# Optimization experiments

Measured on AMD Instinct MI355X. Metric: run time of the kernel, lower is better.

Reference implementation:

```python
import jax, jax.numpy as jnp
import numpy as np
import math

HIDDEN = 1024
HEADS = 16
D_K = HIDDEN // HEADS
D_FF = 4 * HIDDEN
EPS = 1e-5


def gelu_tanh(x):
    # exact match of the module's hand-written GELU
    c = math.sqrt(2.0 / math.pi)
    return 0.5 * x * (1.0 + jnp.tanh(c * (x + 0.044715 * x ** 3)))


def layer_norm(x, gamma, beta):
    mu = jnp.mean(x, axis=-1, keepdims=True)
    var = jnp.mean((x - mu) ** 2, axis=-1, keepdims=True)
    return (x - mu) * jax.lax.rsqrt(var + EPS) * gamma + beta


def setup_inputs() -> dict:
    key = jax.random.key(0)
    ks = jax.random.split(key, 16)
    s = 0.02
    B, S, H = 4, 2048, HIDDEN
    return {
        "x": jax.random.normal(ks[0], (B, S, H), dtype=jnp.float32),
        "Wq": jax.random.normal(ks[1], (H, H), dtype=jnp.float32) * s,
        "bq": jnp.zeros((H,), jnp.float32),
        "Wk": jax.random.normal(ks[2], (H, H), dtype=jnp.float32) * s,
        "bk": jnp.zeros((H,), jnp.float32),
        "Wv": jax.random.normal(ks[3], (H, H), dtype=jnp.float32) * s,
        "bv": jnp.zeros((H,), jnp.float32),
        "Wo": jax.random.normal(ks[4], (H, H), dtype=jnp.float32) * s,
        "bo": jnp.zeros((H,), jnp.float32),
        "W1": jax.random.normal(ks[5], (H, D_FF), dtype=jnp.float32) * s,
        "b1": jnp.zeros((D_FF,), jnp.float32),
        "W2": jax.random.normal(ks[6], (D_FF, H), dtype=jnp.float32) * s,
        "b2": jnp.zeros((H,), jnp.float32),
        "g1": jnp.ones((H,), jnp.float32),
        "be1": jnp.zeros((H,), jnp.float32),
        "g2": jnp.ones((H,), jnp.float32),
        "be2": jnp.zeros((H,), jnp.float32),
    }


def reference(x, Wq, bq, Wk, bk, Wv, bv, Wo, bo, W1, b1, W2, b2, g1, be1, g2, be2):
    B, S, H = x.shape
    # QKV projections -> [B, heads, S, d_k]
    def split_heads(t):
        return t.reshape(B, S, HEADS, D_K).transpose(0, 2, 1, 3)
    q = split_heads(x @ Wq + bq)
    k = split_heads(x @ Wk + bk)
    v = split_heads(x @ Wv + bv)
    scores = jnp.einsum("bhsd,bhtd->bhst", q, k) / math.sqrt(D_K)
    attn = jax.nn.softmax(scores, axis=-1)
    ctx = jnp.einsum("bhst,bhtd->bhsd", attn, v)
    ctx = ctx.transpose(0, 2, 1, 3).reshape(B, S, H)
    attn_out = ctx @ Wo + bo
    x = layer_norm(x + attn_out, g1, be1)
    ff = gelu_tanh(x @ W1 + b1) @ W2 + b2
    x = layer_norm(x + ff, g2, be2)
    return x
```

## Files before the change

kernel.cpp:

```cpp
#include <hip/hip_runtime.h>
#include <hip/hip_bf16.h>
#include <math.h>

#define HIDDEN 1024
#define NHEADS 16
#define DK 64
#define DFF 4096
#define SEQ 2048
#define NBATCH 4
#define NTOK (NBATCH*SEQ)

typedef __attribute__((ext_vector_type(8))) short bf16x8;
typedef __attribute__((ext_vector_type(4))) float f32x4;
typedef __attribute__((ext_vector_type(16))) float f32x16;
typedef __attribute__((ext_vector_type(4))) unsigned short us4;
typedef __attribute__((ext_vector_type(2))) unsigned int u32x2;

typedef __attribute__((address_space(1))) void gvoid;
typedef __attribute__((address_space(3))) void lvoid;

__device__ __forceinline__ unsigned short f2b(float f) {
  union { float f; unsigned int u; } v; v.f = f;
  unsigned int u = v.u;
  return (unsigned short)((u + 0x7fffu + ((u >> 16) & 1u)) >> 16);
}

__device__ __forceinline__ unsigned pack_bf16(float lo, float hi) {
  float2 f2; f2.x = lo; f2.y = hi;
  __hip_bfloat162 h = __float22bfloat162_rn(f2);
  union { __hip_bfloat162 h; unsigned u; } c; c.h = h;
  return c.u;
}

__device__ __forceinline__ void gload_lds16(const void* g, void* l) {
  __builtin_amdgcn_global_load_lds((gvoid*)g, (lvoid*)l, 16, 0, 0);
}

__global__ void k_cvt(const float* __restrict__ in, unsigned short* __restrict__ out, int n4) {
  int i = blockIdx.x * blockDim.x + threadIdx.x;
  int stride = gridDim.x * blockDim.x;
  for (; i < n4; i += stride) {
    float4 v = ((const float4*)in)[i];
    us4 o;
    o.x = f2b(v.x); o.y = f2b(v.y); o.z = f2b(v.z); o.w = f2b(v.w);
    ((us4*)out)[i] = o;
  }
}

__global__ void k_transcvt(const float* __restrict__ W, unsigned short* __restrict__ WT,
                           int K, int N) {
  __shared__ unsigned short tile[64][80];
  int t = threadIdx.x;
  int k0 = blockIdx.x * 64, n0 = blockIdx.y * 64;
  int lr = t >> 2, c0 = (t & 3) * 16;
  const float* src = W + (size_t)(k0 + lr) * N + n0 + c0;
  #pragma unroll
  for (int j = 0; j < 16; ++j) tile[lr][c0 + j] = f2b(src[j]);
  __syncthreads();
  unsigned short* dst = WT + (size_t)(n0 + lr) * K + k0 + c0;
  #pragma unroll
  for (int j = 0; j < 16; ++j) dst[j] = tile[c0 + j][lr];
}

__global__ void k_vtrans(const unsigned short* __restrict__ V, unsigned short* __restrict__ VT) {
  __shared__ unsigned short tile[64][80];
  int bid = blockIdx.x;
  int st = bid & 31, bh = bid >> 5;
  int s0 = st * 64;
  int t = threadIdx.x;
  int lr = t >> 2, c0 = (t & 3) * 16;
  const unsigned short* src = V + (size_t)bh * SEQ * DK + (size_t)(s0 + lr) * DK + c0;
  #pragma unroll
  for (int j = 0; j < 16; ++j) tile[lr][c0 + j] = src[j];
  __syncthreads();
  unsigned short* dst = VT + (size_t)bh * DK * SEQ + (size_t)lr * SEQ + s0 + c0;
  #pragma unroll
  for (int j = 0; j < 16; ++j) dst[j] = tile[c0 + j][lr];
}

template <int MODE>
__global__ __launch_bounds__(256)
void k_gemm(const unsigned short* __restrict__ A, const unsigned short* __restrict__ Bt,
            const float* __restrict__ bias, void* __restrict__ Cout,
            int M, int N, int K) {
  __shared__ __align__(1024) char lds[32768];
  const int tid = threadIdx.x;
  const int lane = tid & 63;
  const int wid = tid >> 6;
  const int wm = wid >> 1, wn = wid & 1;
  const int l15 = lane & 15, lg = lane >> 4;
  const int bm = blockIdx.x, bn = blockIdx.y;

  f32x4 acc[4][4] = {};

  const char* Ab = (const char*)A + (size_t)bm * 128 * (size_t)K * 2;
  const char* Bb = (const char*)Bt + (size_t)bn * 128 * (size_t)K * 2;
  const size_t ldr = (size_t)K * 2;

  for (int k0 = 0; k0 < K; k0 += 64) {
    #pragma unroll
    for (int r = 0; r < 4; ++r) {
      int li = tid * 16 + r * 4096;
      int row = li >> 7;
      int col = (li & 127) ^ ((row & 7) << 4);
      gload_lds16(Ab + (size_t)row * ldr + k0 * 2 + col, lds + li);
      gload_lds16(Bb + (size_t)row * ldr + k0 * 2 + col, lds + 16384 + li);
    }
    __syncthreads();
    #pragma unroll
    for (int kc = 0; kc < 2; ++kc) {
      bf16x8 af[4], bfr[4];
      #pragma unroll
      for (int i = 0; i < 4; ++i) {
        int kb = kc * 64 + (lg << 4);
        int lr = wm * 64 + i * 16 + l15;
        af[i] = *(const bf16x8*)(lds + lr * 128 + (kb ^ ((lr & 7) << 4)));
        int lr2 = wn * 64 + i * 16 + l15;
        bfr[i] = *(const bf16x8*)(lds + 16384 + lr2 * 128 + (kb ^ ((lr2 & 7) << 4)));
      }
      #pragma unroll
      for (int mi = 0; mi < 4; ++mi)
        #pragma unroll
        for (int ni = 0; ni < 4; ++ni)
          acc[mi][ni] = __builtin_amdgcn_mfma_f32_16x16x32_bf16(af[mi], bfr[ni], acc[mi][ni], 0, 0, 0);
    }
    __syncthreads();
  }

  const int mbase = bm * 128 + wm * 64;
  const int nbase = bn * 128 + wn * 64;
  #pragma unroll
  for (int ni = 0; ni < 4; ++ni) {
    int n = nbase + ni * 16 + l15;
    float bv = bias[n];
    #pragma unroll
    for (int mi = 0; mi < 4; ++mi) {
      #pragma unroll
      for (int r = 0; r < 4; ++r) {
        int m = mbase + mi * 16 + lg * 4 + r;
        float val = acc[mi][ni][r] + bv;
        if (MODE == 0) {
          int b = m >> 11, s = m & 2047;
          int h = n >> 6, d = n & 63;
          ((unsigned short*)Cout)[((size_t)(b * NHEADS + h) * SEQ + s) * DK + d] = f2b(val);
        } else if (MODE == 1) {
          ((float*)Cout)[(size_t)m * N + n] = val;
        } else {
          float x = val;
          float t = tanhf(0.7978845608028654f * (x + 0.044715f * x * x * x));
          ((unsigned short*)Cout)[(size_t)m * N + n] = f2b(0.5f * x * (1.0f + t));
        }
      }
    }
  }
}

__global__ __launch_bounds__(256)
void k_attn(const unsigned short* __restrict__ Qp, const unsigned short* __restrict__ Kp,
            const unsigned short* __restrict__ VTp, unsigned short* __restrict__ ctx) {
  const int tid = threadIdx.x, w = tid >> 6, lane = tid & 63;
  const int l31 = lane & 31, hi = lane >> 5;
  const int bid = blockIdx.x;
  const int qb = bid & 15, bh = bid >> 4;
  const size_t base = (size_t)bh * SEQ * DK;
  const size_t baseT = (size_t)bh * DK * SEQ;
  const int q0 = qb * 128 + w * 32;

  bf16x8 qf[4];
  #pragma unroll
  for (int sl = 0; sl < 4; ++sl)
    qf[sl] = *(const bf16x8*)(Qp + base + (size_t)(q0 + l31) * DK + sl * 16 + hi * 8);

  bf16x8 kf[4];
  #pragma unroll
  for (int sl = 0; sl < 4; ++sl)
    kf[sl] = *(const bf16x8*)(Kp + base + (size_t)l31 * DK + sl * 16 + hi * 8);

  float m_run = -1e30f, l_run = 0.f;
  f32x16 o0 = {}, o1 = {};

  for (int kv0 = 0; kv0 < SEQ; kv0 += 32) {
    f32x16 s = {};
    #pragma unroll
    for (int sl = 0; sl < 4; ++sl)
      s = __builtin_amdgcn_mfma_f32_32x32x16_bf16(kf[sl], qf[sl], s, 0, 0, 0);

    int kvn = kv0 + 32;
    if (kvn < SEQ) {
      #pragma unroll
      for (int sl = 0; sl < 4; ++sl)
        kf[sl] = *(const bf16x8*)(Kp + base + (size_t)(kvn + l31) * DK + sl * 16 + hi * 8);
    }
    bf16x8 vf00 = *(const bf16x8*)(VTp + baseT + (size_t)(l31) * SEQ + kv0 + hi * 8);
    bf16x8 vf01 = *(const bf16x8*)(VTp + baseT + (size_t)(l31) * SEQ + kv0 + 16 + hi * 8);
    bf16x8 vf10 = *(const bf16x8*)(VTp + baseT + (size_t)(32 + l31) * SEQ + kv0 + hi * 8);
    bf16x8 vf11 = *(const bf16x8*)(VTp + baseT + (size_t)(32 + l31) * SEQ + kv0 + 16 + hi * 8);

    float mx = fmaxf(s[0], s[1]);
    #pragma unroll
    for (int r = 2; r < 16; ++r) mx = fmaxf(mx, s[r]);
    mx = fmaxf(mx, __shfl_xor(mx, 32));
    float mnew = fmaxf(m_run, mx * 0.125f);
    float corr = __expf(m_run - mnew);
    float p[16];
    float sum = 0.f;
    #pragma unroll
    for (int r = 0; r < 16; ++r) { p[r] = __expf(s[r] * 0.125f - mnew); sum += p[r]; }
    sum += __shfl_xor(sum, 32);
    l_run = l_run * corr + sum;
    m_run = mnew;
    #pragma unroll
    for (int r = 0; r < 16; ++r) { o0[r] *= corr; o1[r] *= corr; }

    unsigned wds[8];
    #pragma unroll
    for (int g = 0; g < 2; ++g) {
      unsigned w0 = pack_bf16(p[g*8+0], p[g*8+1]);
      unsigned w1 = pack_bf16(p[g*8+2], p[g*8+3]);
      unsigned w2 = pack_bf16(p[g*8+4], p[g*8+5]);
      unsigned w3 = pack_bf16(p[g*8+6], p[g*8+7]);
#if __has_builtin(__builtin_amdgcn_permlane32_swap)
      u32x2 r02 = __builtin_amdgcn_permlane32_swap(w0, w2, false, false);
      u32x2 r13 = __builtin_amdgcn_permlane32_swap(w1, w3, false, false);
      wds[g*4+0] = r02.x; wds[g*4+1] = r13.x;
      wds[g*4+2] = r02.y; wds[g*4+3] = r13.y;
#else
      unsigned s0 = __shfl_xor(w0, 32), s1 = __shfl_xor(w1, 32);
      unsigned s2 = __shfl_xor(w2, 32), s3 = __shfl_xor(w3, 32);
      wds[g*4+0] = hi ? s2 : w0; wds[g*4+1] = hi ? s3 : w1;
      wds[g*4+2] = hi ? w2 : s0; wds[g*4+3] = hi ? w3 : s1;
#endif
    }
    union { unsigned u[4]; bf16x8 v; } pb0, pb1;
    pb0.u[0]=wds[0]; pb0.u[1]=wds[1]; pb0.u[2]=wds[2]; pb0.u[3]=wds[3];
    pb1.u[0]=wds[4]; pb1.u[1]=wds[5]; pb1.u[2]=wds[6]; pb1.u[3]=wds[7];

    o0 = __builtin_amdgcn_mfma_f32_32x32x16_bf16(vf00, pb0.v, o0, 0, 0, 0);
    o1 = __builtin_amdgcn_mfma_f32_32x32x16_bf16(vf10, pb0.v, o1, 0, 0, 0);
    o0 = __builtin_amdgcn_mfma_f32_32x32x16_bf16(vf01, pb1.v, o0, 0, 0, 0);
    o1 = __builtin_amdgcn_mfma_f32_32x32x16_bf16(vf11, pb1.v, o1, 0, 0, 0);
  }

  float inv = 1.f / l_run;
  const int b = bh >> 4, h = bh & 15;
  const int q = q0 + l31;
  size_t rowbase = ((size_t)(b * SEQ + q)) * HIDDEN + h * 64;
  #pragma unroll
  for (int g = 0; g < 4; ++g) {
    us4 st0, st1;
    st0.x = f2b(o0[4*g+0] * inv); st0.y = f2b(o0[4*g+1] * inv);
    st0.z = f2b(o0[4*g+2] * inv); st0.w = f2b(o0[4*g+3] * inv);
    st1.x = f2b(o1[4*g+0] * inv); st1.y = f2b(o1[4*g+1] * inv);
    st1.z = f2b(o1[4*g+2] * inv); st1.w = f2b(o1[4*g+3] * inv);
    int d0 = g * 8 + hi * 4;
    *(us4*)(ctx + rowbase + d0)      = st0;
    *(us4*)(ctx + rowbase + 32 + d0) = st1;
  }
}

__global__ __launch_bounds__(256)
void k_ln(const float* __restrict__ a, const float* __restrict__ b,
          const float* __restrict__ gamma, const float* __restrict__ beta,
          float* __restrict__ outf, unsigned short* __restrict__ outb) {
  int row = blockIdx.x;
  int tid = threadIdx.x;
  const float4* A = (const float4*)(a + (size_t)row * HIDDEN);
  const float4* B = (const float4*)(b + (size_t)row * HIDDEN);
  float4 va = A[tid], vb = B[tid];
  float x0 = va.x + vb.x, x1 = va.y + vb.y, x2 = va.z + vb.z, x3 = va.w + vb.w;
  float sum = x0 + x1 + x2 + x3;
  float sq = x0 * x0 + x1 * x1 + x2 * x2 + x3 * x3;
  #pragma unroll
  for (int d = 1; d < 64; d <<= 1) { sum += __shfl_xor(sum, d); sq += __shfl_xor(sq, d); }
  __shared__ float red[8];
  if ((tid & 63) == 0) { red[(tid >> 6) * 2] = sum; red[(tid >> 6) * 2 + 1] = sq; }
  __syncthreads();
  sum = red[0] + red[2] + red[4] + red[6];
  sq  = red[1] + red[3] + red[5] + red[7];
  float mu = sum * (1.f / HIDDEN);
  float var = sq * (1.f / HIDDEN) - mu * mu;
  float rs = rsqrtf(var + 1e-5f);
  float4 g = ((const float4*)gamma)[tid];
  float4 be = ((const float4*)beta)[tid];
  float y0 = (x0 - mu) * rs * g.x + be.x;
  float y1 = (x1 - mu) * rs * g.y + be.y;
  float y2 = (x2 - mu) * rs * g.z + be.z;
  float y3 = (x3 - mu) * rs * g.w + be.w;
  if (outf) { float4 o; o.x = y0; o.y = y1; o.z = y2; o.w = y3; ((float4*)(outf + (size_t)row * HIDDEN))[tid] = o; }
  if (outb) { us4 o; o.x = f2b(y0); o.y = f2b(y1); o.z = f2b(y2); o.w = f2b(y3); ((us4*)(outb + (size_t)row * HIDDEN))[tid] = o; }
}

#define OFF_XB   ((size_t)0)
#define OFF_WQT  ((size_t)16777216)
#define OFF_WKT  ((size_t)18874368)
#define OFF_WVT  ((size_t)20971520)
#define OFF_WOT  ((size_t)23068672)
#define OFF_W1T  ((size_t)25165824)
#define OFF_W2T  ((size_t)33554432)
#define OFF_Q    ((size_t)41943040)
#define OFF_K    ((size_t)58720256)
#define OFF_V    ((size_t)75497472)
#define OFF_VT   ((size_t)92274688)
#define OFF_AO   ((size_t)109051904)
#define OFF_LN1F ((size_t)142606336)

extern "C" void kernel_launch(void* const* d_in, const int* in_sizes, int n_in,
                              void* d_out, int out_size, void* d_ws, size_t ws_size,
                              hipStream_t stream) {
  const float* x   = (const float*)d_in[0];
  const float* Wq  = (const float*)d_in[1];
  const float* bq  = (const float*)d_in[2];
  const float* Wk  = (const float*)d_in[3];
  const float* bk  = (const float*)d_in[4];
  const float* Wv  = (const float*)d_in[5];
  const float* bv  = (const float*)d_in[6];
  const float* Wo  = (const float*)d_in[7];
  const float* bo  = (const float*)d_in[8];
  const float* W1  = (const float*)d_in[9];
  const float* b1  = (const float*)d_in[10];
  const float* W2  = (const float*)d_in[11];
  const float* b2  = (const float*)d_in[12];
  const float* g1  = (const float*)d_in[13];
  const float* be1 = (const float*)d_in[14];
  const float* g2  = (const float*)d_in[15];
  const float* be2 = (const float*)d_in[16];

  char* ws = (char*)d_ws;
  unsigned short* xb   = (unsigned short*)(ws + OFF_XB);
  unsigned short* wqT  = (unsigned short*)(ws + OFF_WQT);
  unsigned short* wkT  = (unsigned short*)(ws + OFF_WKT);
  unsigned short* wvT  = (unsigned short*)(ws + OFF_WVT);
  unsigned short* woT  = (unsigned short*)(ws + OFF_WOT);
  unsigned short* w1T  = (unsigned short*)(ws + OFF_W1T);
  unsigned short* w2T  = (unsigned short*)(ws + OFF_W2T);
  unsigned short* Qb   = (unsigned short*)(ws + OFF_Q);
  unsigned short* Kb   = (unsigned short*)(ws + OFF_K);
  unsigned short* Vb   = (unsigned short*)(ws + OFF_V);
  unsigned short* VTb  = (unsigned short*)(ws + OFF_VT);
  unsigned short* ctx  = (unsigned short*)(ws + OFF_V);
  float*          ao   = (float*)(ws + OFF_AO);
  float*          ln1f = (float*)(ws + OFF_LN1F);
  unsigned short* ln1b = (unsigned short*)(ws + OFF_XB);
  unsigned short* ff1  = (unsigned short*)(ws + OFF_Q);
  float*          ff2  = (float*)(ws + OFF_AO);

  k_cvt<<<2048, 256, 0, stream>>>(x, xb, NTOK * HIDDEN / 4);

  k_transcvt<<<dim3(16, 16), 256, 0, stream>>>(Wq, wqT, 1024, 1024);
  k_transcvt<<<dim3(16, 16), 256, 0, stream>>>(Wk, wkT, 1024, 1024);
  k_transcvt<<<dim3(16, 16), 256, 0, stream>>>(Wv, wvT, 1024, 1024);
  k_transcvt<<<dim3(16, 16), 256, 0, stream>>>(Wo, woT, 1024, 1024);
  k_transcvt<<<dim3(16, 64), 256, 0, stream>>>(W1, w1T, 1024, 4096);
  k_transcvt<<<dim3(64, 16), 256, 0, stream>>>(W2, w2T, 4096, 1024);

  k_gemm<0><<<dim3(64, 8), 256, 0, stream>>>(xb, wqT, bq, Qb, NTOK, HIDDEN, HIDDEN);
  k_gemm<0><<<dim3(64, 8), 256, 0, stream>>>(xb, wkT, bk, Kb, NTOK, HIDDEN, HIDDEN);
  k_gemm<0><<<dim3(64, 8), 256, 0, stream>>>(xb, wvT, bv, Vb, NTOK, HIDDEN, HIDDEN);

  k_vtrans<<<2048, 256, 0, stream>>>(Vb, VTb);

  k_attn<<<1024, 256, 0, stream>>>(Qb, Kb, VTb, ctx);

  k_gemm<1><<<dim3(64, 8), 256, 0, stream>>>(ctx, woT, bo, ao, NTOK, HIDDEN, HIDDEN);

  k_ln<<<NTOK, 256, 0, stream>>>(x, ao, g1, be1, ln1f, ln1b);

  k_gemm<2><<<dim3(64, 32), 256, 0, stream>>>(ln1b, w1T, b1, ff1, NTOK, DFF, HIDDEN);

  k_gemm<1><<<dim3(64, 8), 256, 0, stream>>>(ff1, w2T, b2, ff2, NTOK, HIDDEN, DFF);

  k_ln<<<NTOK, 256, 0, stream>>>(ln1f, ff2, g2, be2, (float*)d_out, nullptr);
}
```

Baseline: 698.5 us.

## Fold softmax scale into Wq, use exp2 with lazy rescale in attention

The 1/sqrt(dk) factor is folded into the Q projection weights and bias, so the attention loop no longer multiplies scores by it. Softmax now uses exp2 with a log2e-scaled running max. The output and sum rescale is skipped while the new tile max stays within a threshold of the running max, which removes per-tile corr multiplies on the 32 accumulator registers. It also raises wave priority around the MFMA groups. The lazy threshold lets unnormalised exponentials grow up to about 2^11.5, which relies on fp32 headroom and slightly changes bf16 rounding of P.

```diff
diff --git a/kernel.cpp b/kernel.cpp
--- a/kernel.cpp
+++ b/kernel.cpp
@@ -48,14 +48,14 @@
 }
 
 __global__ void k_transcvt(const float* __restrict__ W, unsigned short* __restrict__ WT,
-                           int K, int N) {
+                           int K, int N, float scale) {
   __shared__ unsigned short tile[64][80];
   int t = threadIdx.x;
   int k0 = blockIdx.x * 64, n0 = blockIdx.y * 64;
   int lr = t >> 2, c0 = (t & 3) * 16;
   const float* src = W + (size_t)(k0 + lr) * N + n0 + c0;
   #pragma unroll
-  for (int j = 0; j < 16; ++j) tile[lr][c0 + j] = f2b(src[j]);
+  for (int j = 0; j < 16; ++j) tile[lr][c0 + j] = f2b(src[j] * scale);
   __syncthreads();
   unsigned short* dst = WT + (size_t)(n0 + lr) * K + k0 + c0;
   #pragma unroll
@@ -82,7 +82,7 @@
 __global__ __launch_bounds__(256)
 void k_gemm(const unsigned short* __restrict__ A, const unsigned short* __restrict__ Bt,
             const float* __restrict__ bias, void* __restrict__ Cout,
-            int M, int N, int K) {
+            int M, int N, int K, float bscale) {
   __shared__ __align__(1024) char lds[32768];
   const int tid = threadIdx.x;
   const int lane = tid & 63;
@@ -132,7 +132,7 @@
   #pragma unroll
   for (int ni = 0; ni < 4; ++ni) {
     int n = nbase + ni * 16 + l15;
-    float bv = bias[n];
+    float bv = bias[n] * bscale;
     #pragma unroll
     for (int mi = 0; mi < 4; ++mi) {
       #pragma unroll
@@ -166,6 +166,9 @@
   const size_t baseT = (size_t)bh * DK * SEQ;
   const int q0 = qb * 128 + w * 32;
 
+  const float L2E = 1.4426950408889634f;
+  const float THR = 11.541560327111708f;
+
   bf16x8 qf[4];
   #pragma unroll
   for (int sl = 0; sl < 4; ++sl)
@@ -176,14 +179,16 @@
   for (int sl = 0; sl < 4; ++sl)
     kf[sl] = *(const bf16x8*)(Kp + base + (size_t)l31 * DK + sl * 16 + hi * 8);
 
-  float m_run = -1e30f, l_run = 0.f;
+  float M = -1e30f, l_run = 0.f;
   f32x16 o0 = {}, o1 = {};
 
   for (int kv0 = 0; kv0 < SEQ; kv0 += 32) {
     f32x16 s = {};
+    __builtin_amdgcn_s_setprio(1);
     #pragma unroll
     for (int sl = 0; sl < 4; ++sl)
       s = __builtin_amdgcn_mfma_f32_32x32x16_bf16(kf[sl], qf[sl], s, 0, 0, 0);
+    __builtin_amdgcn_s_setprio(0);
 
     int kvn = kv0 + 32;
     if (kvn < SEQ) {
@@ -200,17 +205,24 @@
     #pragma unroll
     for (int r = 2; r < 16; ++r) mx = fmaxf(mx, s[r]);
     mx = fmaxf(mx, __shfl_xor(mx, 32));
-    float mnew = fmaxf(m_run, mx * 0.125f);
-    float corr = __expf(m_run - mnew);
+    float mxl = mx * L2E;
+    if (!__all(mxl <= M + THR)) {
+      float Mnew = fmaxf(M, mxl);
+      float corr = __builtin_amdgcn_exp2f(M - Mnew);
+      l_run *= corr;
+      #pragma unroll
+      for (int r = 0; r < 16; ++r) { o0[r] *= corr; o1[r] *= corr; }
+      M = Mnew;
+    }
     float p[16];
     float sum = 0.f;
     #pragma unroll
-    for (int r = 0; r < 16; ++r) { p[r] = __expf(s[r] * 0.125f - mnew); sum += p[r]; }
+    for (int r = 0; r < 16; ++r) {
+      p[r] = __builtin_amdgcn_exp2f(fmaf(s[r], L2E, -M));
+      sum += p[r];
+    }
     sum += __shfl_xor(sum, 32);
-    l_run = l_run * corr + sum;
-    m_run = mnew;
-    #pragma unroll
-    for (int r = 0; r < 16; ++r) { o0[r] *= corr; o1[r] *= corr; }
+    l_run += sum;
 
     unsigned wds[8];
     #pragma unroll
@@ -235,10 +247,12 @@
     pb0.u[0]=wds[0]; pb0.u[1]=wds[1]; pb0.u[2]=wds[2]; pb0.u[3]=wds[3];
     pb1.u[0]=wds[4]; pb1.u[1]=wds[5]; pb1.u[2]=wds[6]; pb1.u[3]=wds[7];
 
+    __builtin_amdgcn_s_setprio(1);
     o0 = __builtin_amdgcn_mfma_f32_32x32x16_bf16(vf00, pb0.v, o0, 0, 0, 0);
     o1 = __builtin_amdgcn_mfma_f32_32x32x16_bf16(vf10, pb0.v, o1, 0, 0, 0);
     o0 = __builtin_amdgcn_mfma_f32_32x32x16_bf16(vf01, pb1.v, o0, 0, 0, 0);
     o1 = __builtin_amdgcn_mfma_f32_32x32x16_bf16(vf11, pb1.v, o1, 0, 0, 0);
+    __builtin_amdgcn_s_setprio(0);
   }
 
   float inv = 1.f / l_run;
@@ -346,28 +360,28 @@
 
   k_cvt<<<2048, 256, 0, stream>>>(x, xb, NTOK * HIDDEN / 4);
 
-  k_transcvt<<<dim3(16, 16), 256, 0, stream>>>(Wq, wqT, 1024, 1024);
-  k_transcvt<<<dim3(16, 16), 256, 0, stream>>>(Wk, wkT, 1024, 1024);
-  k_transcvt<<<dim3(16, 16), 256, 0, stream>>>(Wv, wvT, 1024, 1024);
-  k_transcvt<<<dim3(16, 16), 256, 0, stream>>>(Wo, woT, 1024, 1024);
-  k_transcvt<<<dim3(16, 64), 256, 0, stream>>>(W1, w1T, 1024, 4096);
-  k_transcvt<<<dim3(64, 16), 256, 0, stream>>>(W2, w2T, 4096, 1024);
-
-  k_gemm<0><<<dim3(64, 8), 256, 0, stream>>>(xb, wqT, bq, Qb, NTOK, HIDDEN, HIDDEN);
-  k_gemm<0><<<dim3(64, 8), 256, 0, stream>>>(xb, wkT, bk, Kb, NTOK, HIDDEN, HIDDEN);
-  k_gemm<0><<<dim3(64, 8), 256, 0, stream>>>(xb, wvT, bv, Vb, NTOK, HIDDEN, HIDDEN);
+  k_transcvt<<<dim3(16, 16), 256, 0, stream>>>(Wq, wqT, 1024, 1024, 0.125f);
+  k_transcvt<<<dim3(16, 16), 256, 0, stream>>>(Wk, wkT, 1024, 1024, 1.0f);
+  k_transcvt<<<dim3(16, 16), 256, 0, stream>>>(Wv, wvT, 1024, 1024, 1.0f);
+  k_transcvt<<<dim3(16, 16), 256, 0, stream>>>(Wo, woT, 1024, 1024, 1.0f);
+  k_transcvt<<<dim3(16, 64), 256, 0, stream>>>(W1, w1T, 1024, 4096, 1.0f);
+  k_transcvt<<<dim3(64, 16), 256, 0, stream>>>(W2, w2T, 4096, 1024, 1.0f);
+
+  k_gemm<0><<<dim3(64, 8), 256, 0, stream>>>(xb, wqT, bq, Qb, NTOK, HIDDEN, HIDDEN, 0.125f);
+  k_gemm<0><<<dim3(64, 8), 256, 0, stream>>>(xb, wkT, bk, Kb, NTOK, HIDDEN, HIDDEN, 1.0f);
+  k_gemm<0><<<dim3(64, 8), 256, 0, stream>>>(xb, wvT, bv, Vb, NTOK, HIDDEN, HIDDEN, 1.0f);
 
   k_vtrans<<<2048, 256, 0, stream>>>(Vb, VTb);
 
   k_attn<<<1024, 256, 0, stream>>>(Qb, Kb, VTb, ctx);
 
-  k_gemm<1><<<dim3(64, 8), 256, 0, stream>>>(ctx, woT, bo, ao, NTOK, HIDDEN, HIDDEN);
+  k_gemm<1><<<dim3(64, 8), 256, 0, stream>>>(ctx, woT, bo, ao, NTOK, HIDDEN, HIDDEN, 1.0f);
 
   k_ln<<<NTOK, 256, 0, stream>>>(x, ao, g1, be1, ln1f, ln1b);
 
-  k_gemm<2><<<dim3(64, 32), 256, 0, stream>>>(ln1b, w1T, b1, ff1, NTOK, DFF, HIDDEN);
-
-  k_gemm<1><<<dim3(64, 8), 256, 0, stream>>>(ff1, w2T, b2, ff2, NTOK, HIDDEN, DFF);
+  k_gemm<2><<<dim3(64, 32), 256, 0, stream>>>(ln1b, w1T, b1, ff1, NTOK, DFF, HIDDEN, 1.0f);
+
+  k_gemm<1><<<dim3(64, 8), 256, 0, stream>>>(ff1, w2T, b2, ff2, NTOK, HIDDEN, DFF, 1.0f);
 
   k_ln<<<NTOK, 256, 0, stream>>>(ln1f, ff2, g2, be2, (float*)d_out, nullptr);
 }
```

Result: slower. 752.9 us (+7.8%).
